# Optimization experiments

Hardware: AMD Instinct MI355X
Metric: run time of the kernel (lower is better)

Reference implementation:

```python
import jax, jax.numpy as jnp
import numpy as np

H, HKV, D, W = 64, 8, 64, 128          # heads, kv heads, head_dim, sliding window
G = H // HKV                            # query heads per kv head
HID = 2880
THETA = 150000.0
SCALE = D ** -0.5
NEG = -1e30


def _rope(x, positions):
    # x: [B,S,h,D]; GPT-NeoX style rotate_half RoPE
    half = D // 2
    inv_freq = 1.0 / (THETA ** (jnp.arange(0, half, dtype=jnp.float32) / half))
    ang = positions.astype(jnp.float32)[:, None] * inv_freq          # [S, D/2]
    cos = jnp.cos(ang)[None, :, None, :]
    sin = jnp.sin(ang)[None, :, None, :]
    x1, x2 = x[..., :half], x[..., half:]
    return jnp.concatenate([x1 * cos - x2 * sin, x2 * cos + x1 * sin], axis=-1)


def setup_inputs() -> dict:
    key = jax.random.key(0)
    ks = jax.random.split(key, 6)
    B, S = 1, 2048
    return {
        "hidden_states": jax.random.normal(ks[0], (B, S, HID), jnp.float32),
        "positions": jnp.arange(S, dtype=jnp.int32),
        "w_qkv": jax.random.normal(ks[1], (HID, (H + 2 * HKV) * D), jnp.float32) * 0.02,
        "b_qkv": jax.random.normal(ks[2], ((H + 2 * HKV) * D,), jnp.float32) * 0.02,
        "w_o": jax.random.normal(ks[3], (H * D, HID), jnp.float32) * 0.02,
        "b_o": jax.random.normal(ks[4], (HID,), jnp.float32) * 0.02,
        "sinks": jax.random.normal(ks[5], (H,), jnp.float32),
    }


def reference(hidden_states, positions, w_qkv, b_qkv, w_o, b_o, sinks):
    B, S, _ = hidden_states.shape
    qkv = hidden_states @ w_qkv + b_qkv                               # [B,S,(H+2Hkv)*D]
    q, k, v = jnp.split(qkv, [H * D, H * D + HKV * D], axis=-1)
    Q = q.reshape(B, S, H, D)
    K = k.reshape(B, S, HKV, D)
    V = v.reshape(B, S, HKV, D)
    Q = _rope(Q, positions)
    K = _rope(K, positions)

    # banded (sliding-window) key/value gather: query i sees keys i-W+1..i
    offsets = jnp.arange(W) - (W - 1)                                 # [-(W-1)..0]
    kidx = jnp.arange(S)[:, None] + offsets                           # [S,W]
    valid = kidx >= 0
    kidx = jnp.maximum(kidx, 0)
    Kw = K[:, kidx]                                                    # [B,S,W,HKV,D]
    Vw = V[:, kidx]

    Qr = Q.reshape(B, S, HKV, G, D)                                    # GQA grouping
    scores = jnp.einsum('bskgd,bswkd->bskgw', Qr, Kw) * SCALE          # [B,S,HKV,G,W]
    scores = jnp.where(valid[None, :, None, None, :], scores, NEG)

    sink = sinks.reshape(HKV, G)[None, None]                           # [1,1,HKV,G]
    m = jnp.maximum(scores.max(axis=-1), sink)                         # [B,S,HKV,G]
    p = jnp.exp(scores - m[..., None])
    denom = p.sum(axis=-1) + jnp.exp(sink - m)                         # sink in normalizer
    out = jnp.einsum('bskgw,bswkd->bskgd', p, Vw) / denom[..., None]

    out = out.reshape(B, S, H * D)
    return out @ w_o + b_o
```

## Files before the change

kernel.cpp:

```cpp
#include <hip/hip_runtime.h>

typedef unsigned short u16;
typedef __bf16 bf16x8 __attribute__((ext_vector_type(8)));
typedef float f32x4 __attribute__((ext_vector_type(4)));
typedef unsigned short u16x8 __attribute__((ext_vector_type(8)));

#define QKV_N 5120
#define SEQ 2048
#define ATTN_K 4096
#define KPAD 2944
#define SCALE 0.125f
#define NEGINF -1e30f

__device__ __forceinline__ u16 f2bf(float f) {
  unsigned int u = __builtin_bit_cast(unsigned int, f);
  u = (u + 0x7FFFu + ((u >> 16) & 1u)) >> 16;
  return (u16)u;
}
__device__ __forceinline__ float bf2f(u16 u) {
  unsigned int x = ((unsigned int)u) << 16;
  return __builtin_bit_cast(float, x);
}

#define MFMA16(a, b, c) __builtin_amdgcn_mfma_f32_16x16x32_bf16((a), (b), (c), 0, 0, 0)

__device__ __forceinline__ void gl_lds16(const u16* g, u16* l) {
  __builtin_amdgcn_global_load_lds(
      (const __attribute__((address_space(1))) unsigned int*)(const void*)g,
      (__attribute__((address_space(3))) unsigned int*)(void*)l, 16, 0, 0);
}

__device__ __forceinline__ bf16x8 fragrd(const u16* base, int row, int rb) {
  return *(const bf16x8*)((const char*)(base + row * 32) + rb);
}

__device__ __forceinline__ bf16x8 lds_frag(const u16* mat, int row, int kh, int lg) {
  int off = row * 128 + ((kh * 64 + lg * 16) ^ ((row & 7) << 4));
  return *(const bf16x8*)((const char*)mat + off);
}

__global__ __launch_bounds__(256) void k_rope_table(const int* __restrict__ pos,
                                                    float2* __restrict__ tab) {
  int t = blockIdx.x * 256 + threadIdx.x;
  int s = t >> 5, i = t & 31;
  float freq = powf(150000.0f, -(float)i * (1.0f / 32.0f));
  float ang = (float)pos[s] * freq;
  float sv, cv;
  sincosf(ang, &sv, &cv);
  tab[t] = make_float2(cv, sv);
}

__global__ __launch_bounds__(256) void k_convert_pad(const float* __restrict__ in,
                                                     u16* __restrict__ out) {
  int i = blockIdx.x * 256 + threadIdx.x;
  int r = i / 736, c4 = i - r * 736;
  if (r >= 2048) return;
  ushort4 o = {0, 0, 0, 0};
  if (c4 < 720) {
    float4 v = *(const float4*)(in + (size_t)r * 2880 + c4 * 4);
    o.x = f2bf(v.x); o.y = f2bf(v.y); o.z = f2bf(v.z); o.w = f2bf(v.w);
  }
  ((ushort4*)out)[(size_t)r * 736 + c4] = o;
}

__global__ __launch_bounds__(256) void k_transpose(const float* __restrict__ in,
                                                   u16* __restrict__ out,
                                                   int Kin, int Kout, int Nd, int Npad) {
  __shared__ float tile[32][33];
  int n0 = blockIdx.x * 32, k0 = blockIdx.y * 32;
  int c = threadIdx.x & 31, r0 = threadIdx.x >> 5;
#pragma unroll
  for (int j = 0; j < 4; j++) {
    int r = r0 + j * 8;
    float v = 0.f;
    if (n0 + c < Nd && k0 + r < Kin) v = in[(size_t)(k0 + r) * Nd + n0 + c];
    tile[r][c] = v;
  }
  __syncthreads();
#pragma unroll
  for (int j = 0; j < 4; j++) {
    int rr = r0 + j * 8;
    int n = n0 + rr;
    if (n < Npad) out[(size_t)n * Kout + k0 + c] = f2bf(tile[c][rr]);
  }
}

__global__ __launch_bounds__(256, 2) void k_gemm1(const u16* __restrict__ Ag,
                                                  const u16* __restrict__ Bg,
                                                  const float* __restrict__ bias,
                                                  u16* __restrict__ C) {
  __shared__ u16 lds_[2][18432];
  u16* L = &lds_[0][0];
  const int tid = threadIdx.x;
  const int lane = tid & 63, wave = tid >> 6;
  const int wm = wave >> 1, wn = wave & 1;
  const int lr = lane & 15, lg = lane >> 4;
  const int bid = blockIdx.x;
  const int xcd = bid & 7, j = bid >> 3;
  const int m0 = (j >> 2) * 128;
  const int n0 = (xcd * 4 + (j & 3)) * 160;

  f32x4 acc[4][5] = {};
  bf16x8 Bf[5], Af0, Af1;

  const int rb = (lg * 16) ^ (((lr >> 1) & 3) << 4);
  const int arow = tid >> 2;
  const int axs = ((tid & 3) ^ ((tid >> 3) & 3)) << 3;

  size_t boff[5];
#pragma unroll
  for (int r_ = 0; r_ < 5; r_++) {
    int e = r_ * 2048 + tid * 8;
    int bkh = (e >= 5120) ? 1 : 0;
    int re = e - bkh * 5120;
    int brow = re >> 5;
    int bch = (re >> 3) & 3;
    int bps = bch ^ ((brow >> 1) & 3);
    boff[r_] = (size_t)(n0 + brow) * KPAD + bkh * 32 + bps * 8;
  }

#define STA(b, kh, kt, r_)                                                      \
  gl_lds16(Ag + (size_t)(m0 + (r_) * 64 + arow) * KPAD + (kt) + (kh) * 32 + axs, \
           L + (b) * 18432 + (kh) * 4096 + (r_) * 2048 + wave * 512)
#define STB(b, kt, r_)                                                          \
  gl_lds16(Bg + boff[r_] + (kt), L + (b) * 18432 + 8192 + (r_) * 2048 + wave * 512)
#define RDB(b, kh)                                                              \
  { _Pragma("unroll") for (int nf = 0; nf < 5; nf++)                            \
      Bf[nf] = fragrd(L + (b) * 18432 + 8192 + (kh) * 5120,                     \
                      wn * 80 + nf * 16 + lr, rb); }
#define RDA(b, kh, mf0_)                                                        \
  { Af0 = fragrd(L + (b) * 18432 + (kh) * 4096, wm * 64 + (mf0_) * 16 + lr, rb); \
    Af1 = fragrd(L + (b) * 18432 + (kh) * 4096, wm * 64 + ((mf0_) + 1) * 16 + lr, rb); }
#define MM(ma, mb)                                                              \
  { __builtin_amdgcn_s_setprio(1);                                              \
    _Pragma("unroll") for (int nf = 0; nf < 5; nf++) {                          \
      acc[ma][nf] = MFMA16(Af0, Bf[nf], acc[ma][nf]);                           \
      acc[mb][nf] = MFMA16(Af1, Bf[nf], acc[mb][nf]); }                         \
    __builtin_amdgcn_s_setprio(0); }
#define BAR __builtin_amdgcn_s_barrier();
#define VM4 asm volatile("s_waitcnt vmcnt(4)" ::: "memory");
#define VM0 asm volatile("s_waitcnt vmcnt(0)" ::: "memory");

  STA(0, 0, 0, 0); STA(0, 0, 0, 1);
  STB(0, 0, 0); STB(0, 0, 1); STB(0, 0, 2); STB(0, 0, 3); STB(0, 0, 4);
  STA(0, 1, 0, 0); STA(0, 1, 0, 1);
  VM4 BAR

  for (int t = 0; t < 46; t++) {
    const int b = t & 1, nb = b ^ 1;
    const int kt1 = (t + 1) * 64;
    const bool st = (t < 45);
    RDB(b, 0) RDA(b, 0, 0)
    if (st) { STA(nb, 0, kt1, 0); STA(nb, 0, kt1, 1); STB(nb, kt1, 0); }
    BAR MM(0, 1) BAR
    RDA(b, 0, 2)
    if (st) { STB(nb, kt1, 1); STB(nb, kt1, 2); VM4 } else { VM0 }
    BAR MM(2, 3) BAR
    RDB(b, 1) RDA(b, 1, 0)
    if (st) { STB(nb, kt1, 3); STB(nb, kt1, 4); }
    BAR MM(0, 1) BAR
    RDA(b, 1, 2)
    if (st) { STA(nb, 1, kt1, 0); STA(nb, 1, kt1, 1); VM4 }
    BAR MM(2, 3) BAR
  }
#undef STA
#undef STB
#undef RDB
#undef RDA
#undef MM
#undef BAR
#undef VM4
#undef VM0

#pragma unroll
  for (int mf = 0; mf < 4; mf++)
#pragma unroll
    for (int nf = 0; nf < 5; nf++) {
      int col = n0 + wn * 80 + nf * 16 + lr;
      float bv = bias[col];
#pragma unroll
      for (int rg = 0; rg < 4; rg++) {
        int row = m0 + wm * 64 + mf * 16 + lg * 4 + rg;
        C[(size_t)row * QKV_N + col] = f2bf(acc[mf][nf][rg] + bv);
      }
    }
}

__global__ __launch_bounds__(256, 2) void k_gemm2(const u16* __restrict__ Ag,
                                                  const u16* __restrict__ Bg,
                                                  const float* __restrict__ bias,
                                                  float* __restrict__ C) {
  __shared__ u16 ldsbuf[2][16384];
  const int tid = threadIdx.x;
  const int lane = tid & 63, wave = tid >> 6;
  const int wm = wave >> 1, wn = wave & 1;
  const int lr = lane & 15, lg = lane >> 4;
  int bid = blockIdx.x;
  int sb = (bid & 7) * 46 + (bid >> 3);
  const int m0 = (sb / 23) * 128, n0 = (sb % 23) * 128;

  f32x4 acc[4][4] = {};

  const int srow = wave * 8 + (lane >> 3);
  const int sc = ((lane & 7) ^ (lane >> 3)) << 3;
  const u16* gA = Ag + (size_t)(m0 + srow) * ATTN_K + sc;
  const u16* gB = Bg + (size_t)(n0 + srow) * ATTN_K + sc;

#define G2_STAGE(kt, b)                                                          \
  {                                                                              \
    u16* Ab = &ldsbuf[b][0];                                                     \
    u16* Bb = &ldsbuf[b][8192];                                                  \
    _Pragma("unroll") for (int r = 0; r < 4; r++) {                              \
      gl_lds16(gA + (size_t)(r * 32) * ATTN_K + (kt), Ab + (r * 32 + wave * 8) * 64); \
      gl_lds16(gB + (size_t)(r * 32) * ATTN_K + (kt), Bb + (r * 32 + wave * 8) * 64); \
    }                                                                            \
  }

  G2_STAGE(0, 0)
  G2_STAGE(64, 1)
  asm volatile("s_waitcnt vmcnt(8)" ::: "memory");
  __builtin_amdgcn_s_barrier();

  for (int t = 0; t < 64; t++) {
    const int b = t & 1;
    const u16* La = &ldsbuf[b][0];
    const u16* Lb = &ldsbuf[b][8192];
    bf16x8 Bf[4][2];
#pragma unroll
    for (int nf = 0; nf < 4; nf++)
#pragma unroll
      for (int kh = 0; kh < 2; kh++)
        Bf[nf][kh] = lds_frag(Lb, wn * 64 + nf * 16 + lr, kh, lg);
    bf16x8 Af[2][2];
#pragma unroll
    for (int mi = 0; mi < 2; mi++)
#pragma unroll
      for (int kh = 0; kh < 2; kh++)
        Af[mi][kh] = lds_frag(La, wm * 64 + mi * 16 + lr, kh, lg);
#pragma unroll
    for (int q = 0; q < 2; q++) {
      bf16x8 An[2][2];
      if (q < 1) {
#pragma unroll
        for (int mi = 0; mi < 2; mi++)
#pragma unroll
          for (int kh = 0; kh < 2; kh++)
            An[mi][kh] = lds_frag(La, wm * 64 + ((q + 1) * 2 + mi) * 16 + lr, kh, lg);
      }
      __builtin_amdgcn_s_setprio(1);
#pragma unroll
      for (int mi = 0; mi < 2; mi++)
#pragma unroll
        for (int nf = 0; nf < 4; nf++)
#pragma unroll
          for (int kh = 0; kh < 2; kh++)
            acc[q * 2 + mi][nf] = MFMA16(Af[mi][kh], Bf[nf][kh], acc[q * 2 + mi][nf]);
      __builtin_amdgcn_s_setprio(0);
      if (q < 1) {
#pragma unroll
        for (int mi = 0; mi < 2; mi++)
#pragma unroll
          for (int kh = 0; kh < 2; kh++)
            Af[mi][kh] = An[mi][kh];
      }
    }
    __builtin_amdgcn_s_barrier();
    if (t <= 61) {
      G2_STAGE((t + 2) * 64, b)
      asm volatile("s_waitcnt vmcnt(8)" ::: "memory");
    } else {
      asm volatile("s_waitcnt vmcnt(0)" ::: "memory");
    }
    __builtin_amdgcn_s_barrier();
  }
#undef G2_STAGE

#pragma unroll
  for (int mi = 0; mi < 4; mi++)
#pragma unroll
    for (int ni = 0; ni < 4; ni++) {
      int row = m0 + wm * 64 + mi * 16 + lg * 4;
      int col = n0 + wn * 64 + ni * 16 + lr;
      if (col < 2880) {
        float bv = bias[col];
#pragma unroll
        for (int rg = 0; rg < 4; rg++)
          C[(size_t)(row + rg) * 2880 + col] = acc[mi][ni][rg] + bv;
      }
    }
}

__global__ __launch_bounds__(1024, 1) void k_attn(const u16* __restrict__ qkv,
                                                  const float* __restrict__ sinks,
                                                  const float2* __restrict__ tab,
                                                  u16* __restrict__ out) {
  __shared__ u16 Klds[192 * 64];
  __shared__ u16 Vt[64 * 200];
  __shared__ u16 Pslab[16 * 32 * 40];
  const int hk = blockIdx.y;
  const int s0 = blockIdx.x * 64;
  const int kb = s0 - 127;
  const int tid = threadIdx.x;
  const int lane = tid & 63, w = tid >> 6;
  const int lr = lane & 15, lg = lane >> 4;
  const int head = hk * 8 + (w & 7);
  const int qoff = (w >> 3) * 32;

  if (tid < 768) {
    int key = tid >> 2, c = tid & 3;
    int kidx = kb + key;
    u16x8 v1 = {0, 0, 0, 0, 0, 0, 0, 0}, v2 = v1;
    if (kidx >= 0 && kidx < SEQ) {
      const u16* base = qkv + (size_t)kidx * QKV_N + 4096 + hk * 64;
      u16x8 x1 = *(const u16x8*)(base + c * 8);
      u16x8 x2 = *(const u16x8*)(base + 32 + c * 8);
      const float2* cs = tab + (size_t)kidx * 32 + c * 8;
#pragma unroll
      for (int j = 0; j < 8; j++) {
        float f1 = bf2f(x1[j]), f2 = bf2f(x2[j]);
        float2 t = cs[j];
        v1[j] = f2bf(f1 * t.x - f2 * t.y);
        v2[j] = f2bf(f2 * t.x + f1 * t.y);
      }
    }
    int o1 = (key * 128 + c * 16) ^ ((key & 7) << 4);
    int o2 = (key * 128 + (c + 4) * 16) ^ ((key & 7) << 4);
    *(u16x8*)((char*)Klds + o1) = v1;
    *(u16x8*)((char*)Klds + o2) = v2;
  }
  for (int e4 = tid; e4 < 192 * 16; e4 += 1024) {
    int key = e4 >> 4, d0 = (e4 & 15) * 4;
    int kidx = kb + key;
    ushort4 v = {0, 0, 0, 0};
    if (kidx >= 0 && kidx < SEQ)
      v = *(const ushort4*)(qkv + (size_t)kidx * QKV_N + 4608 + hk * 64 + d0);
    Vt[(d0 + 0) * 200 + key] = v.x;
    Vt[(d0 + 1) * 200 + key] = v.y;
    Vt[(d0 + 2) * 200 + key] = v.z;
    Vt[(d0 + 3) * 200 + key] = v.w;
  }

  bf16x8 qf[2][2];
#pragma unroll
  for (int rt = 0; rt < 2; rt++) {
    int s = s0 + qoff + rt * 16 + lr;
    const u16* base = qkv + (size_t)s * QKV_N + head * 64 + lg * 8;
    u16x8 r0 = *(const u16x8*)(base);
    u16x8 r1 = *(const u16x8*)(base + 32);
    const float2* cs = tab + (size_t)s * 32 + lg * 8;
    u16x8 y0, y1;
#pragma unroll
    for (int j = 0; j < 8; j++) {
      float f1 = bf2f(r0[j]), f2 = bf2f(r1[j]);
      float2 t = cs[j];
      y0[j] = f2bf(f1 * t.x - f2 * t.y);
      y1[j] = f2bf(f2 * t.x + f1 * t.y);
    }
    qf[rt][0] = __builtin_bit_cast(bf16x8, y0);
    qf[rt][1] = __builtin_bit_cast(bf16x8, y1);
  }
  __syncthreads();

  f32x4 sc[2][10];
  f32x4 zz = {0.f, 0.f, 0.f, 0.f};
#pragma unroll
  for (int rt = 0; rt < 2; rt++)
#pragma unroll
    for (int nt = 0; nt < 10; nt++) sc[rt][nt] = zz;
#pragma unroll
  for (int nt = 0; nt < 10; nt++) {
    int key = qoff + nt * 16 + lr;
#pragma unroll
    for (int ks = 0; ks < 2; ks++) {
      int off = (key * 128 + ks * 64 + lg * 16) ^ ((key & 7) << 4);
      bf16x8 kf = *(const bf16x8*)((const char*)Klds + off);
      sc[0][nt] = MFMA16(qf[0][ks], kf, sc[0][nt]);
      sc[1][nt] = MFMA16(qf[1][ks], kf, sc[1][nt]);
    }
  }

#pragma unroll
  for (int rt = 0; rt < 2; rt++)
#pragma unroll
    for (int nt = 0; nt < 10; nt++)
#pragma unroll
      for (int rg = 0; rg < 4; rg++) {
        int qq = rt * 16 + lg * 4 + rg;
        int jl = nt * 16 + lr;
        bool valid = (jl >= qq) && (jl <= qq + 127) && ((kb + qoff + jl) >= 0);
        sc[rt][nt][rg] = valid ? sc[rt][nt][rg] * SCALE : NEGINF;
      }

  const float sink = sinks[head];
  float den[2][4];
#pragma unroll
  for (int rt = 0; rt < 2; rt++)
#pragma unroll
    for (int rg = 0; rg < 4; rg++) {
      float m = NEGINF;
#pragma unroll
      for (int nt = 0; nt < 10; nt++) m = fmaxf(m, sc[rt][nt][rg]);
#pragma unroll
      for (int x = 1; x < 16; x <<= 1) m = fmaxf(m, __shfl_xor(m, x, 64));
      m = fmaxf(m, sink);
      float sum = 0.f;
#pragma unroll
      for (int nt = 0; nt < 10; nt++) {
        float p = __expf(sc[rt][nt][rg] - m);
        sc[rt][nt][rg] = p;
        sum += p;
      }
#pragma unroll
      for (int x = 1; x < 16; x <<= 1) sum += __shfl_xor(sum, x, 64);
      den[rt][rg] = sum + __expf(sink - m);
    }

  f32x4 oacc[2][4];
#pragma unroll
  for (int rt = 0; rt < 2; rt++)
#pragma unroll
    for (int dn = 0; dn < 4; dn++) oacc[rt][dn] = zz;
  u16* slab = &Pslab[w * 32 * 40];
#pragma unroll
  for (int kt = 0; kt < 5; kt++) {
#pragma unroll
    for (int rt = 0; rt < 2; rt++)
#pragma unroll
      for (int j2 = 0; j2 < 2; j2++)
#pragma unroll
        for (int rg = 0; rg < 4; rg++)
          slab[(rt * 16 + lg * 4 + rg) * 40 + j2 * 16 + lr] = f2bf(sc[rt][kt * 2 + j2][rg]);
    asm volatile("s_waitcnt lgkmcnt(0)" ::: "memory");
    __builtin_amdgcn_sched_barrier(0);
    bf16x8 pf0 = *(const bf16x8*)&slab[lr * 40 + lg * 8];
    bf16x8 pf1 = *(const bf16x8*)&slab[(16 + lr) * 40 + lg * 8];
#pragma unroll
    for (int dn = 0; dn < 4; dn++) {
      bf16x8 vf = *(const bf16x8*)&Vt[(dn * 16 + lr) * 200 + qoff + kt * 32 + lg * 8];
      oacc[0][dn] = MFMA16(pf0, vf, oacc[0][dn]);
      oacc[1][dn] = MFMA16(pf1, vf, oacc[1][dn]);
    }
  }

#pragma unroll
  for (int rt = 0; rt < 2; rt++)
#pragma unroll
    for (int dn = 0; dn < 4; dn++)
#pragma unroll
      for (int rg = 0; rg < 4; rg++) {
        int s = s0 + qoff + rt * 16 + lg * 4 + rg;
        float val = oacc[rt][dn][rg] / den[rt][rg];
        out[(size_t)s * ATTN_K + head * 64 + dn * 16 + lr] = f2bf(val);
      }
}

extern "C" void kernel_launch(void* const* d_in, const int* in_sizes, int n_in,
                              void* d_out, int out_size, void* d_ws, size_t ws_size,
                              hipStream_t stream) {
  const float* hs = (const float*)d_in[0];
  const int* pos = (const int*)d_in[1];
  const float* wqkv = (const float*)d_in[2];
  const float* bqkv = (const float*)d_in[3];
  const float* wo = (const float*)d_in[4];
  const float* bo = (const float*)d_in[5];
  const float* sinks = (const float*)d_in[6];
  float* out = (float*)d_out;

  char* ws = (char*)d_ws;
  u16* qkvb = (u16*)(ws + 0);
  u16* hsb = (u16*)(ws + 41943040);
  u16* wqkvT = (u16*)(ws + 54001664);
  u16* attnb = (u16*)(ws + 41943040);
  u16* woT = (u16*)(ws + 84148224);
  float2* tab = (float2*)(ws + 108265472);

  k_rope_table<<<256, 256, 0, stream>>>(pos, tab);
  k_convert_pad<<<5888, 256, 0, stream>>>(hs, hsb);
  k_transpose<<<dim3(160, 92), 256, 0, stream>>>(wqkv, wqkvT, 2880, KPAD, 5120, 5120);
  k_transpose<<<dim3(92, 128), 256, 0, stream>>>(wo, woT, 4096, 4096, 2880, 2944);
  k_gemm1<<<512, 256, 0, stream>>>(hsb, wqkvT, bqkv, qkvb);
  k_attn<<<dim3(32, 8), 1024, 0, stream>>>(qkvb, sinks, tab, attnb);
  k_gemm2<<<368, 256, 0, stream>>>(attnb, woT, bo, out);
}
```

Measured before the change: 202.9 us.

## Fuse prep kernels, retile output GEMM to 128x96, halve attention block size

Merges the RoPE table, input conversion and both weight transposes into one launch dispatched by block index, which removes three kernel launches. The output GEMM switches from 128x128 tiles (368 blocks) to 128x96 tiles (480 blocks), so the N=2880 edge divides evenly and more CUs are filled. Attention blocks drop from 1024 to 512 threads, with each wave looping over two 32-query slices, so two blocks can share a CU. The trade-off is less K/V LDS reuse per wave-instant and a serial loop inside each wave.

```diff
diff --git a/kernel.cpp b/kernel.cpp
--- a/kernel.cpp
+++ b/kernel.cpp
@@ -39,49 +39,64 @@
   return *(const bf16x8*)((const char*)mat + off);
 }
 
-__global__ __launch_bounds__(256) void k_rope_table(const int* __restrict__ pos,
-                                                    float2* __restrict__ tab) {
-  int t = blockIdx.x * 256 + threadIdx.x;
-  int s = t >> 5, i = t & 31;
-  float freq = powf(150000.0f, -(float)i * (1.0f / 32.0f));
-  float ang = (float)pos[s] * freq;
-  float sv, cv;
-  sincosf(ang, &sv, &cv);
-  tab[t] = make_float2(cv, sv);
-}
-
-__global__ __launch_bounds__(256) void k_convert_pad(const float* __restrict__ in,
-                                                     u16* __restrict__ out) {
-  int i = blockIdx.x * 256 + threadIdx.x;
-  int r = i / 736, c4 = i - r * 736;
-  if (r >= 2048) return;
-  ushort4 o = {0, 0, 0, 0};
-  if (c4 < 720) {
-    float4 v = *(const float4*)(in + (size_t)r * 2880 + c4 * 4);
-    o.x = f2bf(v.x); o.y = f2bf(v.y); o.z = f2bf(v.z); o.w = f2bf(v.w);
-  }
-  ((ushort4*)out)[(size_t)r * 736 + c4] = o;
-}
-
-__global__ __launch_bounds__(256) void k_transpose(const float* __restrict__ in,
-                                                   u16* __restrict__ out,
-                                                   int Kin, int Kout, int Nd, int Npad) {
+__global__ __launch_bounds__(256) void k_prep(const int* __restrict__ pos,
+                                              float2* __restrict__ tab,
+                                              const float* __restrict__ hs,
+                                              u16* __restrict__ hsb,
+                                              const float* __restrict__ wqkv,
+                                              u16* __restrict__ wqkvT,
+                                              const float* __restrict__ wo,
+                                              u16* __restrict__ woT) {
   __shared__ float tile[32][33];
-  int n0 = blockIdx.x * 32, k0 = blockIdx.y * 32;
-  int c = threadIdx.x & 31, r0 = threadIdx.x >> 5;
-#pragma unroll
-  for (int j = 0; j < 4; j++) {
-    int r = r0 + j * 8;
-    float v = 0.f;
-    if (n0 + c < Nd && k0 + r < Kin) v = in[(size_t)(k0 + r) * Nd + n0 + c];
-    tile[r][c] = v;
-  }
-  __syncthreads();
-#pragma unroll
-  for (int j = 0; j < 4; j++) {
-    int rr = r0 + j * 8;
-    int n = n0 + rr;
-    if (n < Npad) out[(size_t)n * Kout + k0 + c] = f2bf(tile[c][rr]);
+  const int blk = blockIdx.x;
+  if (blk < 256) {
+    int t = blk * 256 + threadIdx.x;
+    int s = t >> 5, i = t & 31;
+    float freq = powf(150000.0f, -(float)i * (1.0f / 32.0f));
+    float ang = (float)pos[s] * freq;
+    float sv, cv;
+    sincosf(ang, &sv, &cv);
+    tab[t] = make_float2(cv, sv);
+  } else if (blk < 6144) {
+    int i = (blk - 256) * 256 + threadIdx.x;
+    int r = i / 736, c4 = i - r * 736;
+    if (r < 2048) {
+      ushort4 o = {0, 0, 0, 0};
+      if (c4 < 720) {
+        float4 v = *(const float4*)(hs + (size_t)r * 2880 + c4 * 4);
+        o.x = f2bf(v.x); o.y = f2bf(v.y); o.z = f2bf(v.z); o.w = f2bf(v.w);
+      }
+      ((ushort4*)hsb)[(size_t)r * 736 + c4] = o;
+    }
+  } else {
+    const float* in;
+    u16* out;
+    int Kin, Kout, Nd, Npad, bx, by;
+    if (blk < 20864) {
+      int q = blk - 6144;
+      bx = q % 160; by = q / 160;
+      in = wqkv; out = wqkvT; Kin = 2880; Kout = KPAD; Nd = 5120; Npad = 5120;
+    } else {
+      int q = blk - 20864;
+      bx = q % 92; by = q / 92;
+      in = wo; out = woT; Kin = 4096; Kout = 4096; Nd = 2880; Npad = 2944;
+    }
+    int n0 = bx * 32, k0 = by * 32;
+    int c = threadIdx.x & 31, r0 = threadIdx.x >> 5;
+#pragma unroll
+    for (int j = 0; j < 4; j++) {
+      int r = r0 + j * 8;
+      float v = 0.f;
+      if (n0 + c < Nd && k0 + r < Kin) v = in[(size_t)(k0 + r) * Nd + n0 + c];
+      tile[r][c] = v;
+    }
+    __syncthreads();
+#pragma unroll
+    for (int j = 0; j < 4; j++) {
+      int rr = r0 + j * 8;
+      int n = n0 + rr;
+      if (n < Npad) out[(size_t)n * Kout + k0 + c] = f2bf(tile[c][rr]);
+    }
   }
 }
 
@@ -168,7 +183,6 @@
 #undef RDB
 #undef RDA
 #undef MM
-#undef BAR
 #undef VM4
 #undef VM0
 
@@ -190,16 +204,16 @@
                                                   const u16* __restrict__ Bg,
                                                   const float* __restrict__ bias,
                                                   float* __restrict__ C) {
-  __shared__ u16 ldsbuf[2][16384];
+  __shared__ u16 ldsbuf[2][14336];
   const int tid = threadIdx.x;
   const int lane = tid & 63, wave = tid >> 6;
   const int wm = wave >> 1, wn = wave & 1;
   const int lr = lane & 15, lg = lane >> 4;
   int bid = blockIdx.x;
-  int sb = (bid & 7) * 46 + (bid >> 3);
-  const int m0 = (sb / 23) * 128, n0 = (sb % 23) * 128;
-
-  f32x4 acc[4][4] = {};
+  int l = (bid & 7) * 60 + (bid >> 3);
+  const int m0 = (l & 15) * 128, n0 = (l >> 4) * 96;
+
+  f32x4 acc[4][3] = {};
 
   const int srow = wave * 8 + (lane >> 3);
   const int sc = ((lane & 7) ^ (lane >> 3)) << 3;
@@ -210,27 +224,27 @@
   {                                                                              \
     u16* Ab = &ldsbuf[b][0];                                                     \
     u16* Bb = &ldsbuf[b][8192];                                                  \
-    _Pragma("unroll") for (int r = 0; r < 4; r++) {                              \
+    _Pragma("unroll") for (int r = 0; r < 4; r++)                                \
       gl_lds16(gA + (size_t)(r * 32) * ATTN_K + (kt), Ab + (r * 32 + wave * 8) * 64); \
+    _Pragma("unroll") for (int r = 0; r < 3; r++)                                \
       gl_lds16(gB + (size_t)(r * 32) * ATTN_K + (kt), Bb + (r * 32 + wave * 8) * 64); \
-    }                                                                            \
   }
 
   G2_STAGE(0, 0)
   G2_STAGE(64, 1)
-  asm volatile("s_waitcnt vmcnt(8)" ::: "memory");
+  asm volatile("s_waitcnt vmcnt(7)" ::: "memory");
   __builtin_amdgcn_s_barrier();
 
   for (int t = 0; t < 64; t++) {
     const int b = t & 1;
     const u16* La = &ldsbuf[b][0];
     const u16* Lb = &ldsbuf[b][8192];
-    bf16x8 Bf[4][2];
-#pragma unroll
-    for (int nf = 0; nf < 4; nf++)
+    bf16x8 Bf[3][2];
+#pragma unroll
+    for (int nf = 0; nf < 3; nf++)
 #pragma unroll
       for (int kh = 0; kh < 2; kh++)
-        Bf[nf][kh] = lds_frag(Lb, wn * 64 + nf * 16 + lr, kh, lg);
+        Bf[nf][kh] = lds_frag(Lb, wn * 48 + nf * 16 + lr, kh, lg);
     bf16x8 Af[2][2];
 #pragma unroll
     for (int mi = 0; mi < 2; mi++)
@@ -251,7 +265,7 @@
 #pragma unroll
       for (int mi = 0; mi < 2; mi++)
 #pragma unroll
-        for (int nf = 0; nf < 4; nf++)
+        for (int nf = 0; nf < 3; nf++)
 #pragma unroll
           for (int kh = 0; kh < 2; kh++)
             acc[q * 2 + mi][nf] = MFMA16(Af[mi][kh], Bf[nf][kh], acc[q * 2 + mi][nf]);
@@ -267,7 +281,7 @@
     __builtin_amdgcn_s_barrier();
     if (t <= 61) {
       G2_STAGE((t + 2) * 64, b)
-      asm volatile("s_waitcnt vmcnt(8)" ::: "memory");
+      asm volatile("s_waitcnt vmcnt(7)" ::: "memory");
     } else {
       asm volatile("s_waitcnt vmcnt(0)" ::: "memory");
     }
@@ -278,36 +292,33 @@
 #pragma unroll
   for (int mi = 0; mi < 4; mi++)
 #pragma unroll
-    for (int ni = 0; ni < 4; ni++) {
+    for (int ni = 0; ni < 3; ni++) {
       int row = m0 + wm * 64 + mi * 16 + lg * 4;
-      int col = n0 + wn * 64 + ni * 16 + lr;
-      if (col < 2880) {
-        float bv = bias[col];
-#pragma unroll
-        for (int rg = 0; rg < 4; rg++)
-          C[(size_t)(row + rg) * 2880 + col] = acc[mi][ni][rg] + bv;
-      }
-    }
-}
-
-__global__ __launch_bounds__(1024, 1) void k_attn(const u16* __restrict__ qkv,
-                                                  const float* __restrict__ sinks,
-                                                  const float2* __restrict__ tab,
-                                                  u16* __restrict__ out) {
+      int col = n0 + wn * 48 + ni * 16 + lr;
+      float bv = bias[col];
+#pragma unroll
+      for (int rg = 0; rg < 4; rg++)
+        C[(size_t)(row + rg) * 2880 + col] = acc[mi][ni][rg] + bv;
+    }
+}
+
+__global__ __launch_bounds__(512, 2) void k_attn(const u16* __restrict__ qkv,
+                                                 const float* __restrict__ sinks,
+                                                 const float2* __restrict__ tab,
+                                                 u16* __restrict__ out) {
   __shared__ u16 Klds[192 * 64];
   __shared__ u16 Vt[64 * 200];
-  __shared__ u16 Pslab[16 * 32 * 40];
+  __shared__ u16 Pslab[8 * 32 * 40];
   const int hk = blockIdx.y;
   const int s0 = blockIdx.x * 64;
   const int kb = s0 - 127;
   const int tid = threadIdx.x;
   const int lane = tid & 63, w = tid >> 6;
   const int lr = lane & 15, lg = lane >> 4;
-  const int head = hk * 8 + (w & 7);
-  const int qoff = (w >> 3) * 32;
-
-  if (tid < 768) {
-    int key = tid >> 2, c = tid & 3;
+  const int head = hk * 8 + w;
+
+  for (int u = tid; u < 192 * 4; u += 512) {
+    int key = u >> 2, c = u & 3;
     int kidx = kb + key;
     u16x8 v1 = {0, 0, 0, 0, 0, 0, 0, 0}, v2 = v1;
     if (kidx >= 0 && kidx < SEQ) {
@@ -316,11 +327,11 @@
       u16x8 x2 = *(const u16x8*)(base + 32 + c * 8);
       const float2* cs = tab + (size_t)kidx * 32 + c * 8;
 #pragma unroll
-      for (int j = 0; j < 8; j++) {
-        float f1 = bf2f(x1[j]), f2 = bf2f(x2[j]);
-        float2 t = cs[j];
-        v1[j] = f2bf(f1 * t.x - f2 * t.y);
-        v2[j] = f2bf(f2 * t.x + f1 * t.y);
+      for (int jj = 0; jj < 8; jj++) {
+        float f1 = bf2f(x1[jj]), f2 = bf2f(x2[jj]);
+        float2 t = cs[jj];
+        v1[jj] = f2bf(f1 * t.x - f2 * t.y);
+        v2[jj] = f2bf(f2 * t.x + f1 * t.y);
       }
     }
     int o1 = (key * 128 + c * 16) ^ ((key & 7) << 4);
@@ -328,7 +339,7 @@
     *(u16x8*)((char*)Klds + o1) = v1;
     *(u16x8*)((char*)Klds + o2) = v2;
   }
-  for (int e4 = tid; e4 < 192 * 16; e4 += 1024) {
+  for (int e4 = tid; e4 < 192 * 16; e4 += 512) {
     int key = e4 >> 4, d0 = (e4 & 15) * 4;
     int kidx = kb + key;
     ushort4 v = {0, 0, 0, 0};
@@ -339,119 +350,126 @@
     Vt[(d0 + 2) * 200 + key] = v.z;
     Vt[(d0 + 3) * 200 + key] = v.w;
   }
-
-  bf16x8 qf[2][2];
-#pragma unroll
-  for (int rt = 0; rt < 2; rt++) {
-    int s = s0 + qoff + rt * 16 + lr;
-    const u16* base = qkv + (size_t)s * QKV_N + head * 64 + lg * 8;
-    u16x8 r0 = *(const u16x8*)(base);
-    u16x8 r1 = *(const u16x8*)(base + 32);
-    const float2* cs = tab + (size_t)s * 32 + lg * 8;
-    u16x8 y0, y1;
-#pragma unroll
-    for (int j = 0; j < 8; j++) {
-      float f1 = bf2f(r0[j]), f2 = bf2f(r1[j]);
-      float2 t = cs[j];
-      y0[j] = f2bf(f1 * t.x - f2 * t.y);
-      y1[j] = f2bf(f2 * t.x + f1 * t.y);
-    }
-    qf[rt][0] = __builtin_bit_cast(bf16x8, y0);
-    qf[rt][1] = __builtin_bit_cast(bf16x8, y1);
-  }
   __syncthreads();
 
-  f32x4 sc[2][10];
+  const float sink = sinks[head];
+  u16* slab = &Pslab[w * 32 * 40];
   f32x4 zz = {0.f, 0.f, 0.f, 0.f};
-#pragma unroll
-  for (int rt = 0; rt < 2; rt++)
-#pragma unroll
-    for (int nt = 0; nt < 10; nt++) sc[rt][nt] = zz;
-#pragma unroll
-  for (int nt = 0; nt < 10; nt++) {
-    int key = qoff + nt * 16 + lr;
-#pragma unroll
-    for (int ks = 0; ks < 2; ks++) {
-      int off = (key * 128 + ks * 64 + lg * 16) ^ ((key & 7) << 4);
-      bf16x8 kf = *(const bf16x8*)((const char*)Klds + off);
-      sc[0][nt] = MFMA16(qf[0][ks], kf, sc[0][nt]);
-      sc[1][nt] = MFMA16(qf[1][ks], kf, sc[1][nt]);
-    }
-  }
-
-#pragma unroll
-  for (int rt = 0; rt < 2; rt++)
-#pragma unroll
-    for (int nt = 0; nt < 10; nt++)
+
+  for (int qs = 0; qs < 2; qs++) {
+    const int qbase = s0 + qs * 32;
+    const int koff = qs * 32;
+
+    bf16x8 qf[2][2];
+#pragma unroll
+    for (int rt = 0; rt < 2; rt++) {
+      int s = qbase + rt * 16 + lr;
+      const u16* base = qkv + (size_t)s * QKV_N + head * 64 + lg * 8;
+      u16x8 r0 = *(const u16x8*)(base);
+      u16x8 r1 = *(const u16x8*)(base + 32);
+      const float2* cs = tab + (size_t)s * 32 + lg * 8;
+      u16x8 y0, y1;
+#pragma unroll
+      for (int jj = 0; jj < 8; jj++) {
+        float f1 = bf2f(r0[jj]), f2 = bf2f(r1[jj]);
+        float2 t = cs[jj];
+        y0[jj] = f2bf(f1 * t.x - f2 * t.y);
+        y1[jj] = f2bf(f2 * t.x + f1 * t.y);
+      }
+      qf[rt][0] = __builtin_bit_cast(bf16x8, y0);
+      qf[rt][1] = __builtin_bit_cast(bf16x8, y1);
+    }
+
+    f32x4 sc[2][10];
+#pragma unroll
+    for (int rt = 0; rt < 2; rt++)
+#pragma unroll
+      for (int nt = 0; nt < 10; nt++) sc[rt][nt] = zz;
+#pragma unroll
+    for (int nt = 0; nt < 10; nt++) {
+      int key = koff + nt * 16 + lr;
+#pragma unroll
+      for (int ks = 0; ks < 2; ks++) {
+        int off = (key * 128 + ks * 64 + lg * 16) ^ ((key & 7) << 4);
+        bf16x8 kf = *(const bf16x8*)((const char*)Klds + off);
+        sc[0][nt] = MFMA16(qf[0][ks], kf, sc[0][nt]);
+        sc[1][nt] = MFMA16(qf[1][ks], kf, sc[1][nt]);
+      }
+    }
+
+#pragma unroll
+    for (int rt = 0; rt < 2; rt++)
+#pragma unroll
+      for (int nt = 0; nt < 10; nt++)
+#pragma unroll
+        for (int rg = 0; rg < 4; rg++) {
+          int qq = rt * 16 + lg * 4 + rg;
+          int jl = nt * 16 + lr;
+          bool valid = (jl >= qq) && (jl <= qq + 127) && ((kb + koff + jl) >= 0);
+          sc[rt][nt][rg] = valid ? sc[rt][nt][rg] * SCALE : NEGINF;
+        }
+
+    float den[2][4];
+#pragma unroll
+    for (int rt = 0; rt < 2; rt++)
 #pragma unroll
       for (int rg = 0; rg < 4; rg++) {
-        int qq = rt * 16 + lg * 4 + rg;
-        int jl = nt * 16 + lr;
-        bool valid = (jl >= qq) && (jl <= qq + 127) && ((kb + qoff + jl) >= 0);
-        sc[rt][nt][rg] = valid ? sc[rt][nt][rg] * SCALE : NEGINF;
-      }
-
-  const float sink = sinks[head];
-  float den[2][4];
-#pragma unroll
-  for (int rt = 0; rt < 2; rt++)
-#pragma unroll
-    for (int rg = 0; rg < 4; rg++) {
-      float m = NEGINF;
-#pragma unroll
-      for (int nt = 0; nt < 10; nt++) m = fmaxf(m, sc[rt][nt][rg]);
-#pragma unroll
-      for (int x = 1; x < 16; x <<= 1) m = fmaxf(m, __shfl_xor(m, x, 64));
-      m = fmaxf(m, sink);
-      float sum = 0.f;
-#pragma unroll
-      for (int nt = 0; nt < 10; nt++) {
-        float p = __expf(sc[rt][nt][rg] - m);
-        sc[rt][nt][rg] = p;
-        sum += p;
-      }
-#pragma unroll
-      for (int x = 1; x < 16; x <<= 1) sum += __shfl_xor(sum, x, 64);
-      den[rt][rg] = sum + __expf(sink - m);
-    }
-
-  f32x4 oacc[2][4];
-#pragma unroll
-  for (int rt = 0; rt < 2; rt++)
-#pragma unroll
-    for (int dn = 0; dn < 4; dn++) oacc[rt][dn] = zz;
-  u16* slab = &Pslab[w * 32 * 40];
-#pragma unroll
-  for (int kt = 0; kt < 5; kt++) {
+        float m = NEGINF;
+#pragma unroll
+        for (int nt = 0; nt < 10; nt++) m = fmaxf(m, sc[rt][nt][rg]);
+#pragma unroll
+        for (int x = 1; x < 16; x <<= 1) m = fmaxf(m, __shfl_xor(m, x, 64));
+        m = fmaxf(m, sink);
+        float sum = 0.f;
+#pragma unroll
+        for (int nt = 0; nt < 10; nt++) {
+          float p = __expf(sc[rt][nt][rg] - m);
+          sc[rt][nt][rg] = p;
+          sum += p;
+        }
+#pragma unroll
+        for (int x = 1; x < 16; x <<= 1) sum += __shfl_xor(sum, x, 64);
+        den[rt][rg] = sum + __expf(sink - m);
+      }
+
+    f32x4 oacc[2][4];
 #pragma unroll
     for (int rt = 0; rt < 2; rt++)
 #pragma unroll
-      for (int j2 = 0; j2 < 2; j2++)
-#pragma unroll
-        for (int rg = 0; rg < 4; rg++)
-          slab[(rt * 16 + lg * 4 + rg) * 40 + j2 * 16 + lr] = f2bf(sc[rt][kt * 2 + j2][rg]);
-    asm volatile("s_waitcnt lgkmcnt(0)" ::: "memory");
-    __builtin_amdgcn_sched_barrier(0);
-    bf16x8 pf0 = *(const bf16x8*)&slab[lr * 40 + lg * 8];
-    bf16x8 pf1 = *(const bf16x8*)&slab[(16 + lr) * 40 + lg * 8];
-#pragma unroll
-    for (int dn = 0; dn < 4; dn++) {
-      bf16x8 vf = *(const bf16x8*)&Vt[(dn * 16 + lr) * 200 + qoff + kt * 32 + lg * 8];
-      oacc[0][dn] = MFMA16(pf0, vf, oacc[0][dn]);
-      oacc[1][dn] = MFMA16(pf1, vf, oacc[1][dn]);
-    }
-  }
-
-#pragma unroll
-  for (int rt = 0; rt < 2; rt++)
-#pragma unroll
-    for (int dn = 0; dn < 4; dn++)
-#pragma unroll
-      for (int rg = 0; rg < 4; rg++) {
-        int s = s0 + qoff + rt * 16 + lg * 4 + rg;
-        float val = oacc[rt][dn][rg] / den[rt][rg];
-        out[(size_t)s * ATTN_K + head * 64 + dn * 16 + lr] = f2bf(val);
-      }
+      for (int dn = 0; dn < 4; dn++) oacc[rt][dn] = zz;
+#pragma unroll
+    for (int kt = 0; kt < 5; kt++) {
+#pragma unroll
+      for (int rt = 0; rt < 2; rt++)
+#pragma unroll
+        for (int j2 = 0; j2 < 2; j2++)
+#pragma unroll
+          for (int rg = 0; rg < 4; rg++)
+            slab[(rt * 16 + lg * 4 + rg) * 40 + j2 * 16 + lr] =
+                f2bf(sc[rt][kt * 2 + j2][rg]);
+      asm volatile("s_waitcnt lgkmcnt(0)" ::: "memory");
+      __builtin_amdgcn_sched_barrier(0);
+      bf16x8 pf0 = *(const bf16x8*)&slab[lr * 40 + lg * 8];
+      bf16x8 pf1 = *(const bf16x8*)&slab[(16 + lr) * 40 + lg * 8];
+#pragma unroll
+      for (int dn = 0; dn < 4; dn++) {
+        bf16x8 vf = *(const bf16x8*)&Vt[(dn * 16 + lr) * 200 + koff + kt * 32 + lg * 8];
+        oacc[0][dn] = MFMA16(pf0, vf, oacc[0][dn]);
+        oacc[1][dn] = MFMA16(pf1, vf, oacc[1][dn]);
+      }
+    }
+
+#pragma unroll
+    for (int rt = 0; rt < 2; rt++)
+#pragma unroll
+      for (int dn = 0; dn < 4; dn++)
+#pragma unroll
+        for (int rg = 0; rg < 4; rg++) {
+          int s = qbase + rt * 16 + lg * 4 + rg;
+          float val = oacc[rt][dn][rg] / den[rt][rg];
+          out[(size_t)s * ATTN_K + head * 64 + dn * 16 + lr] = f2bf(val);
+        }
+  }
 }
 
 extern "C" void kernel_launch(void* const* d_in, const int* in_sizes, int n_in,
@@ -474,11 +492,8 @@
   u16* woT = (u16*)(ws + 84148224);
   float2* tab = (float2*)(ws + 108265472);
 
-  k_rope_table<<<256, 256, 0, stream>>>(pos, tab);
-  k_convert_pad<<<5888, 256, 0, stream>>>(hs, hsb);
-  k_transpose<<<dim3(160, 92), 256, 0, stream>>>(wqkv, wqkvT, 2880, KPAD, 5120, 5120);
-  k_transpose<<<dim3(92, 128), 256, 0, stream>>>(wo, woT, 4096, 4096, 2880, 2944);
+  k_prep<<<32640, 256, 0, stream>>>(pos, tab, hs, hsb, wqkv, wqkvT, wo, woT);
   k_gemm1<<<512, 256, 0, stream>>>(hsb, wqkvT, bqkv, qkvb);
-  k_attn<<<dim3(32, 8), 1024, 0, stream>>>(qkvb, sinks, tab, attnb);
-  k_gemm2<<<368, 256, 0, stream>>>(attnb, woT, bo, out);
-}
+  k_attn<<<dim3(32, 8), 512, 0, stream>>>(qkvb, sinks, tab, attnb);
+  k_gemm2<<<480, 256, 0, stream>>>(attnb, woT, bo, out);
+}
```

Result: faster. 179.8 us (-11.4%).
